# Kernel optimization log

Hardware: AMD Instinct MI355X
Metric: run time of the kernel (lower is better)

Reference implementation:

```python
import jax, jax.numpy as jnp
import numpy as np

N = 8192
F_IN = 128
D = 128
NEG_SLOPE = 0.2  # cfg.negativeslope (standard GAT value)
MASK_FILL = -9e15


def setup_inputs() -> dict:
    key = jax.random.key(0)
    k1, k2, k3, k4 = jax.random.split(key, 4)
    A = jax.random.randint(k1, (N, N), 0, 2, dtype=jnp.int32)
    X = jax.random.normal(k2, (N, F_IN), dtype=jnp.float32)
    # glorot init for Ws, xavier_uniform(gain=1.414) for a
    lim_w = float(np.sqrt(6.0 / (F_IN + D)))
    Ws = jax.random.uniform(k3, (F_IN, D), minval=-lim_w, maxval=lim_w, dtype=jnp.float32)
    lim_a = 1.414 * float(np.sqrt(6.0 / (2 * D + 1)))
    a = jax.random.uniform(k4, (2 * D, 1), minval=-lim_a, maxval=lim_a, dtype=jnp.float32)
    return {"A": A, "X": X, "Ws": Ws, "a": a}


def reference(A, X, Ws, a):
    # Wh: [N, D]
    Wh = X @ Ws
    d = Wh.shape[-1]
    # additive attention: e_ij = leaky_relu(Wh_i . a1 + Wh_j . a2)
    e1 = Wh @ a[:d]          # [N, 1]
    e2 = Wh @ a[d:]          # [N, 1]
    e = jax.nn.leaky_relu(e1 + e2.T, negative_slope=NEG_SLOPE)  # [N, N]
    e = jnp.where(A > 0, e, MASK_FILL)
    attn = jax.nn.softmax(e, axis=1)  # row-wise over neighbors
    H = attn @ Wh            # [N, D]
    return H
```

## Files before the change

### kernel.cpp

```cpp
#include <hip/hip_runtime.h>
#include <hip/hip_bf16.h>

#define NN 8192
#define DD 128

typedef __attribute__((ext_vector_type(8))) short short8;
typedef __attribute__((ext_vector_type(4))) float f32x4;
typedef unsigned int u32;
typedef unsigned long long u64;

__device__ __forceinline__ ushort f2bf(float f) {
    __hip_bfloat16 h = __float2bfloat16(f);
    return *(ushort*)&h;
}
__device__ __forceinline__ u32 asu(float f) {
    union { float f; u32 i; } v; v.f = f; return v.i;
}

__global__ __launch_bounds__(256) void k0_pack(const int* __restrict__ A,
                                               u32* __restrict__ Abits) {
    int t = threadIdx.x;
    size_t base = (size_t)blockIdx.x * 8192 + (size_t)t * 32;
    u32 bits = 0;
#pragma unroll
    for (int j = 0; j < 8; ++j) {
        int4 v = *(const int4*)(A + base + j * 4);
        bits |= (v.x != 0 ? 1u : 0u) << (j * 4 + 0);
        bits |= (v.y != 0 ? 1u : 0u) << (j * 4 + 1);
        bits |= (v.z != 0 ? 1u : 0u) << (j * 4 + 2);
        bits |= (v.w != 0 ? 1u : 0u) << (j * 4 + 3);
    }
    Abits[blockIdx.x * 256 + t] = bits;
}

__global__ __launch_bounds__(256) void k1_fused(
    const float* __restrict__ X, const float* __restrict__ Ws,
    const float* __restrict__ a, ushort* __restrict__ WhT,
    float* __restrict__ Rt, float* __restrict__ E2p, float* __restrict__ E2n) {
    __shared__ float lWs[128 * 132];
    __shared__ float lX[32 * 132];
    __shared__ float la[256];
    int t = threadIdx.x, bx = blockIdx.x;
    int i0 = bx * 32;
    const float4* Ws4 = (const float4*)Ws;
    const float4* X4 = (const float4*)X;
    la[t] = a[t];
    for (int j = 0; j < 16; ++j) {
        int u = j * 256 + t;
        int k = u >> 5, c4 = u & 31;
        *(float4*)&lWs[k * 132 + c4 * 4] = Ws4[u];
    }
    for (int j = 0; j < 4; ++j) {
        int u = j * 256 + t;
        int r = u >> 5, c4 = u & 31;
        *(float4*)&lX[r * 132 + c4 * 4] = X4[bx * 1024 + u];
    }
    __syncthreads();
    int r0 = (t >> 5) * 4, c0 = (t & 31) * 4;
    float acc[4][4];
#pragma unroll
    for (int i = 0; i < 4; ++i)
#pragma unroll
        for (int j = 0; j < 4; ++j) acc[i][j] = 0.f;
#pragma unroll 4
    for (int k = 0; k < 128; ++k) {
        float4 wv = *(const float4*)&lWs[k * 132 + c0];
        float x0 = lX[(r0 + 0) * 132 + k];
        float x1 = lX[(r0 + 1) * 132 + k];
        float x2 = lX[(r0 + 2) * 132 + k];
        float x3 = lX[(r0 + 3) * 132 + k];
#pragma unroll
        for (int j = 0; j < 4; ++j) {
            acc[0][j] += x0 * ((const float*)&wv)[j];
            acc[1][j] += x1 * ((const float*)&wv)[j];
            acc[2][j] += x2 * ((const float*)&wv)[j];
            acc[3][j] += x3 * ((const float*)&wv)[j];
        }
    }
    __syncthreads();
    float* lT = lWs;
#pragma unroll
    for (int i = 0; i < 4; ++i)
#pragma unroll
        for (int j = 0; j < 4; ++j) lT[(c0 + j) * 33 + r0 + i] = acc[i][j];
    __syncthreads();
    if (t < 128) {
        int r = t >> 2, q = t & 3;
        float s1 = 0.f, s2 = 0.f;
        for (int j = 0; j < 32; ++j) {
            int d = q * 32 + j;
            float v = lT[d * 33 + r];
            s1 += v * la[d];
            s2 += v * la[128 + d];
        }
        s1 += __shfl_xor(s1, 1); s1 += __shfl_xor(s1, 2);
        s2 += __shfl_xor(s2, 1); s2 += __shfl_xor(s2, 2);
        if (q == 0) {
            int i = i0 + r;
            Rt[i]  = __expf(-0.8f * s1);
            E2p[i] = __expf(s2);
            E2n[i] = __expf(0.2f * s2);
        }
    }
    int d = t >> 1, hf = t & 1;
    __attribute__((aligned(16))) ushort tmp[16];
#pragma unroll
    for (int s = 0; s < 16; ++s) tmp[s] = f2bf(lT[d * 33 + hf * 16 + s]);
    uint4* dst = (uint4*)&WhT[(size_t)d * NN + i0 + hf * 16];
    const uint4* srcv = (const uint4*)tmp;
    dst[0] = srcv[0];
    dst[1] = srcv[1];
}

__device__ __forceinline__ f32x4 mfma_bf16(short8 a, short8 b, f32x4 c) {
    return __builtin_amdgcn_mfma_f32_16x16x32_bf16(a, b, c, 0, 0, 0);
}

__device__ __forceinline__ void k3_step(
    const short8* Bv, u64 bits, int ko, int kgs,
    const float* lEp, const float* lEn, float ratio, int h, int kg,
    f32x4& acc0, f32x4& acc1, f32x4& acc2, f32x4& acc3, f32x4& accl,
    short8 ones) {
    u32 lo = (u32)bits, hi = (u32)(bits >> 32);
#pragma unroll
    for (int tp = 0; tp < 2; ++tp) {
        int ke = ko + tp * 32 + kg * 8;
        float ep[8], en[8];
        *(float4*)(ep)     = *(const float4*)&lEp[ke];
        *(float4*)(ep + 4) = *(const float4*)&lEp[ke + 4];
        *(float4*)(en)     = *(const float4*)&lEn[ke];
        *(float4*)(en + 4) = *(const float4*)&lEn[ke + 4];
        u32 byte = ((tp ? hi : lo) >> kgs) & 0xFFu;
        u32 wb[8];
#pragma unroll
        for (int u = 0; u < 8; ++u) {
            float w = fmaxf(ep[u], ratio * en[u]);
            w = (byte & (1u << u)) ? w : 0.f;
            wb[u] = asu(w);
        }
        short8 af;
#pragma unroll
        for (int p = 0; p < 4; ++p)
            ((u32*)&af)[p] = __builtin_amdgcn_perm(wb[2 * p + 1], wb[2 * p], 0x07060302);
        acc0 = mfma_bf16(af, Bv[tp * 4 + 0], acc0);
        acc1 = mfma_bf16(af, Bv[tp * 4 + 1], acc1);
        acc2 = mfma_bf16(af, Bv[tp * 4 + 2], acc2);
        acc3 = mfma_bf16(af, Bv[tp * 4 + 3], acc3);
        if (h == 0) accl = mfma_bf16(af, ones, accl);
    }
}

__global__ __launch_bounds__(512, 4) void k3_main(
    const u32* __restrict__ Abits, const ushort* __restrict__ WhT,
    const float* __restrict__ Rt, const float* __restrict__ E2p,
    const float* __restrict__ E2n, float* __restrict__ Hp,
    float* __restrict__ Lp) {

    __shared__ float lEp[2048];
    __shared__ float lEn[2048];

    int tid = threadIdx.x;
    int lane = tid & 63;
    int wv = tid >> 6;
    int g = wv & 3;
    int h = wv >> 2;
    int n = lane & 15;
    int kg = lane >> 4;
    int kgs = kg * 8;

    int bx = blockIdx.x;
    int kb = blockIdx.y;
    int row = bx * 64 + g * 16 + n;
    int kbase = kb * 2048;

#pragma unroll
    for (int j = 0; j < 4; ++j) {
        lEp[tid + j * 512] = E2p[kbase + tid + j * 512];
        lEn[tid + j * 512] = E2n[kbase + tid + j * 512];
    }

    float ratio = Rt[row];
    const u64* Arow = (const u64*)Abits + (size_t)row * 128 + kb * 32;
    const ushort* Bc0 = WhT + (size_t)(h * 64 +  0 + n) * NN + kbase + kgs;
    const ushort* Bc1 = WhT + (size_t)(h * 64 + 16 + n) * NN + kbase + kgs;
    const ushort* Bc2 = WhT + (size_t)(h * 64 + 32 + n) * NN + kbase + kgs;
    const ushort* Bc3 = WhT + (size_t)(h * 64 + 48 + n) * NN + kbase + kgs;

    short8 ones;
#pragma unroll
    for (int j = 0; j < 8; ++j) ones[j] = (short)0x3F80;

    f32x4 acc0 = (f32x4){0.f, 0.f, 0.f, 0.f};
    f32x4 acc1 = (f32x4){0.f, 0.f, 0.f, 0.f};
    f32x4 acc2 = (f32x4){0.f, 0.f, 0.f, 0.f};
    f32x4 acc3 = (f32x4){0.f, 0.f, 0.f, 0.f};
    f32x4 accl = (f32x4){0.f, 0.f, 0.f, 0.f};

    __syncthreads();

    short8 Ba[8], Bb[8];
    u64 bitsA, bitsB;
#define LOADB(Bd, kt_)                                        \
    {   int ko_ = (kt_) * 64;                                 \
        Bd[0] = *(const short8*)(Bc0 + ko_);                  \
        Bd[1] = *(const short8*)(Bc1 + ko_);                  \
        Bd[2] = *(const short8*)(Bc2 + ko_);                  \
        Bd[3] = *(const short8*)(Bc3 + ko_);                  \
        Bd[4] = *(const short8*)(Bc0 + ko_ + 32);             \
        Bd[5] = *(const short8*)(Bc1 + ko_ + 32);             \
        Bd[6] = *(const short8*)(Bc2 + ko_ + 32);             \
        Bd[7] = *(const short8*)(Bc3 + ko_ + 32);             \
    }

    LOADB(Ba, 0);
    bitsA = Arow[0];

    for (int kt = 0; kt < 32; kt += 2) {
        LOADB(Bb, kt + 1);
        bitsB = Arow[kt + 1];
        k3_step(Ba, bitsA, kt * 64, kgs, lEp, lEn, ratio, h, kg,
                acc0, acc1, acc2, acc3, accl, ones);
        int ktn = (kt + 2 < 32) ? kt + 2 : 31;
        LOADB(Ba, ktn);
        bitsA = Arow[ktn];
        k3_step(Bb, bitsB, (kt + 1) * 64, kgs, lEp, lEn, ratio, h, kg,
                acc0, acc1, acc2, acc3, accl, ones);
    }
#undef LOADB

    if (h == 0 && n == 0) {
#pragma unroll
        for (int r = 0; r < 4; ++r)
            Lp[(size_t)kb * NN + bx * 64 + g * 16 + kg * 4 + r] = accl[r];
    }
    float* Hpb = Hp + (size_t)kb * (NN * DD);
#pragma unroll
    for (int r = 0; r < 4; ++r) {
        int orow = bx * 64 + g * 16 + kg * 4 + r;
        Hpb[(size_t)orow * DD + h * 64 + n]      = acc0[r];
        Hpb[(size_t)orow * DD + h * 64 + 16 + n] = acc1[r];
        Hpb[(size_t)orow * DD + h * 64 + 32 + n] = acc2[r];
        Hpb[(size_t)orow * DD + h * 64 + 48 + n] = acc3[r];
    }
}

__global__ void k4_final(const float* __restrict__ Hp, const float* __restrict__ Lp,
                         float* __restrict__ out) {
    int idx = blockIdx.x * 256 + threadIdx.x;
    int i = idx >> 7;
    float sv = Hp[idx] + Hp[1048576 + idx] + Hp[2097152 + idx] + Hp[3145728 + idx];
    float l = Lp[i] + Lp[8192 + i] + Lp[16384 + i] + Lp[24576 + i];
    out[idx] = sv / l;
}

extern "C" void kernel_launch(void* const* d_in, const int* in_sizes, int n_in,
                              void* d_out, int out_size, void* d_ws, size_t ws_size,
                              hipStream_t stream) {
    const int*   A  = (const int*)d_in[0];
    const float* X  = (const float*)d_in[1];
    const float* Ws = (const float*)d_in[2];
    const float* a  = (const float*)d_in[3];
    float* out = (float*)d_out;

    char* ws = (char*)d_ws;
    u32*    Abits = (u32*)(ws);
    ushort* WhT   = (ushort*)(ws + (8u << 20));
    float*  Rt    = (float*)(ws + (10u << 20));
    float*  E2p   = (float*)(ws + (10u << 20) + (32u << 10));
    float*  E2n   = (float*)(ws + (10u << 20) + (64u << 10));
    float*  Lp    = (float*)(ws + (10u << 20) + (96u << 10));
    float*  Hp    = (float*)(ws + (12u << 20));

    k0_pack<<<8192, 256, 0, stream>>>(A, Abits);
    k1_fused<<<256, 256, 0, stream>>>(X, Ws, a, WhT, Rt, E2p, E2n);
    k3_main<<<dim3(128, 4), 512, 0, stream>>>(Abits, WhT, Rt, E2p, E2n, Hp, Lp);
    k4_final<<<4096, 256, 0, stream>>>(Hp, Lp, out);
}
```

Before: 508.9 us.

## Coalesce A packing, pack exp factors as bf16 pairs, re-grid attention kernel

k0_pack now reads A with fully coalesced int4 loads, builds nibbles in shared memory, then assembles 32-bit mask words, with 4x fewer blocks each doing 4x the work. The two exp factor arrays are packed into one u32 of two bf16 values, halving LDS traffic and footprint in the main kernel. The main kernel moves to 256-thread blocks over 32 rows and 1024-column K chunks (256x8 grid) and drops the explicit double-buffered B loads. The final reduce sums 8 partials instead of 4. Risks are more partial-sum traffic, less explicit prefetch, and bf16 rounding of the exp factors.

```diff
diff --git a/kernel.cpp b/kernel.cpp
--- a/kernel.cpp
+++ b/kernel.cpp
@@ -8,6 +8,7 @@
 typedef __attribute__((ext_vector_type(4))) float f32x4;
 typedef unsigned int u32;
 typedef unsigned long long u64;
+typedef unsigned char u8;
 
 __device__ __forceinline__ ushort f2bf(float f) {
     __hip_bfloat16 h = __float2bfloat16(f);
@@ -16,27 +17,41 @@
 __device__ __forceinline__ u32 asu(float f) {
     union { float f; u32 i; } v; v.f = f; return v.i;
 }
+__device__ __forceinline__ float asf(u32 u) {
+    union { u32 i; float f; } v; v.i = u; return v.f;
+}
 
 __global__ __launch_bounds__(256) void k0_pack(const int* __restrict__ A,
                                                u32* __restrict__ Abits) {
+    __shared__ u8 ln[8192];
     int t = threadIdx.x;
-    size_t base = (size_t)blockIdx.x * 8192 + (size_t)t * 32;
-    u32 bits = 0;
-#pragma unroll
-    for (int j = 0; j < 8; ++j) {
-        int4 v = *(const int4*)(A + base + j * 4);
-        bits |= (v.x != 0 ? 1u : 0u) << (j * 4 + 0);
-        bits |= (v.y != 0 ? 1u : 0u) << (j * 4 + 1);
-        bits |= (v.z != 0 ? 1u : 0u) << (j * 4 + 2);
-        bits |= (v.w != 0 ? 1u : 0u) << (j * 4 + 3);
-    }
-    Abits[blockIdx.x * 256 + t] = bits;
+    size_t base4 = (size_t)blockIdx.x * 8192;
+    const int4* A4 = (const int4*)A;
+#pragma unroll
+    for (int j = 0; j < 32; ++j) {
+        int u = j * 256 + t;
+        int4 v = A4[base4 + u];
+        u32 nib = (v.x ? 1u : 0u) | (v.y ? 2u : 0u) | (v.z ? 4u : 0u) | (v.w ? 8u : 0u);
+        ln[u] = (u8)nib;
+    }
+    __syncthreads();
+    const u64* l8 = (const u64*)ln;
+#pragma unroll
+    for (int j = 0; j < 4; ++j) {
+        int w = j * 256 + t;
+        u64 b = l8[w];
+        u32 word = 0;
+#pragma unroll
+        for (int m = 0; m < 8; ++m)
+            word |= ((u32)(b >> (8 * m)) & 0xFu) << (4 * m);
+        Abits[blockIdx.x * 1024 + w] = word;
+    }
 }
 
 __global__ __launch_bounds__(256) void k1_fused(
     const float* __restrict__ X, const float* __restrict__ Ws,
     const float* __restrict__ a, ushort* __restrict__ WhT,
-    float* __restrict__ Rt, float* __restrict__ E2p, float* __restrict__ E2n) {
+    float* __restrict__ Rt, u32* __restrict__ Epack) {
     __shared__ float lWs[128 * 132];
     __shared__ float lX[32 * 132];
     __shared__ float la[256];
@@ -97,9 +112,8 @@
         s2 += __shfl_xor(s2, 1); s2 += __shfl_xor(s2, 2);
         if (q == 0) {
             int i = i0 + r;
-            Rt[i]  = __expf(-0.8f * s1);
-            E2p[i] = __expf(s2);
-            E2n[i] = __expf(0.2f * s2);
+            Rt[i] = __expf(-0.8f * s1);
+            Epack[i] = (u32)f2bf(__expf(s2)) | ((u32)f2bf(__expf(0.2f * s2)) << 16);
         }
     }
     int d = t >> 1, hf = t & 1;
@@ -116,71 +130,32 @@
     return __builtin_amdgcn_mfma_f32_16x16x32_bf16(a, b, c, 0, 0, 0);
 }
 
-__device__ __forceinline__ void k3_step(
-    const short8* Bv, u64 bits, int ko, int kgs,
-    const float* lEp, const float* lEn, float ratio, int h, int kg,
-    f32x4& acc0, f32x4& acc1, f32x4& acc2, f32x4& acc3, f32x4& accl,
-    short8 ones) {
-    u32 lo = (u32)bits, hi = (u32)(bits >> 32);
-#pragma unroll
-    for (int tp = 0; tp < 2; ++tp) {
-        int ke = ko + tp * 32 + kg * 8;
-        float ep[8], en[8];
-        *(float4*)(ep)     = *(const float4*)&lEp[ke];
-        *(float4*)(ep + 4) = *(const float4*)&lEp[ke + 4];
-        *(float4*)(en)     = *(const float4*)&lEn[ke];
-        *(float4*)(en + 4) = *(const float4*)&lEn[ke + 4];
-        u32 byte = ((tp ? hi : lo) >> kgs) & 0xFFu;
-        u32 wb[8];
-#pragma unroll
-        for (int u = 0; u < 8; ++u) {
-            float w = fmaxf(ep[u], ratio * en[u]);
-            w = (byte & (1u << u)) ? w : 0.f;
-            wb[u] = asu(w);
-        }
-        short8 af;
-#pragma unroll
-        for (int p = 0; p < 4; ++p)
-            ((u32*)&af)[p] = __builtin_amdgcn_perm(wb[2 * p + 1], wb[2 * p], 0x07060302);
-        acc0 = mfma_bf16(af, Bv[tp * 4 + 0], acc0);
-        acc1 = mfma_bf16(af, Bv[tp * 4 + 1], acc1);
-        acc2 = mfma_bf16(af, Bv[tp * 4 + 2], acc2);
-        acc3 = mfma_bf16(af, Bv[tp * 4 + 3], acc3);
-        if (h == 0) accl = mfma_bf16(af, ones, accl);
-    }
-}
-
-__global__ __launch_bounds__(512, 4) void k3_main(
+__global__ __launch_bounds__(256, 5) void k3_main(
     const u32* __restrict__ Abits, const ushort* __restrict__ WhT,
-    const float* __restrict__ Rt, const float* __restrict__ E2p,
-    const float* __restrict__ E2n, float* __restrict__ Hp,
-    float* __restrict__ Lp) {
-
-    __shared__ float lEp[2048];
-    __shared__ float lEn[2048];
+    const float* __restrict__ Rt, const u32* __restrict__ Epack,
+    float* __restrict__ Hp, float* __restrict__ Lp) {
+
+    __shared__ u32 lE[1024];
 
     int tid = threadIdx.x;
     int lane = tid & 63;
     int wv = tid >> 6;
-    int g = wv & 3;
-    int h = wv >> 2;
+    int g = wv & 1;
+    int h = wv >> 1;
     int n = lane & 15;
     int kg = lane >> 4;
     int kgs = kg * 8;
 
     int bx = blockIdx.x;
     int kb = blockIdx.y;
-    int row = bx * 64 + g * 16 + n;
-    int kbase = kb * 2048;
-
-#pragma unroll
-    for (int j = 0; j < 4; ++j) {
-        lEp[tid + j * 512] = E2p[kbase + tid + j * 512];
-        lEn[tid + j * 512] = E2n[kbase + tid + j * 512];
-    }
+    int row = bx * 32 + g * 16 + n;
+    int kbase = kb * 1024;
+
+#pragma unroll
+    for (int j = 0; j < 4; ++j) lE[j * 256 + tid] = Epack[kbase + j * 256 + tid];
 
     float ratio = Rt[row];
-    const u64* Arow = (const u64*)Abits + (size_t)row * 128 + kb * 32;
+    const u64* Arow = (const u64*)Abits + (size_t)row * 128 + kb * 16;
     const ushort* Bc0 = WhT + (size_t)(h * 64 +  0 + n) * NN + kbase + kgs;
     const ushort* Bc1 = WhT + (size_t)(h * 64 + 16 + n) * NN + kbase + kgs;
     const ushort* Bc2 = WhT + (size_t)(h * 64 + 32 + n) * NN + kbase + kgs;
@@ -198,45 +173,58 @@
 
     __syncthreads();
 
-    short8 Ba[8], Bb[8];
-    u64 bitsA, bitsB;
-#define LOADB(Bd, kt_)                                        \
-    {   int ko_ = (kt_) * 64;                                 \
-        Bd[0] = *(const short8*)(Bc0 + ko_);                  \
-        Bd[1] = *(const short8*)(Bc1 + ko_);                  \
-        Bd[2] = *(const short8*)(Bc2 + ko_);                  \
-        Bd[3] = *(const short8*)(Bc3 + ko_);                  \
-        Bd[4] = *(const short8*)(Bc0 + ko_ + 32);             \
-        Bd[5] = *(const short8*)(Bc1 + ko_ + 32);             \
-        Bd[6] = *(const short8*)(Bc2 + ko_ + 32);             \
-        Bd[7] = *(const short8*)(Bc3 + ko_ + 32);             \
-    }
-
-    LOADB(Ba, 0);
-    bitsA = Arow[0];
-
-    for (int kt = 0; kt < 32; kt += 2) {
-        LOADB(Bb, kt + 1);
-        bitsB = Arow[kt + 1];
-        k3_step(Ba, bitsA, kt * 64, kgs, lEp, lEn, ratio, h, kg,
-                acc0, acc1, acc2, acc3, accl, ones);
-        int ktn = (kt + 2 < 32) ? kt + 2 : 31;
-        LOADB(Ba, ktn);
-        bitsA = Arow[ktn];
-        k3_step(Bb, bitsB, (kt + 1) * 64, kgs, lEp, lEn, ratio, h, kg,
-                acc0, acc1, acc2, acc3, accl, ones);
-    }
-#undef LOADB
+    u64 bitsA = Arow[0];
+
+    for (int kt = 0; kt < 16; ++kt) {
+        int ko = kt * 64;
+        short8 B0 = *(const short8*)(Bc0 + ko);
+        short8 B1 = *(const short8*)(Bc1 + ko);
+        short8 B2 = *(const short8*)(Bc2 + ko);
+        short8 B3 = *(const short8*)(Bc3 + ko);
+        short8 B4 = *(const short8*)(Bc0 + ko + 32);
+        short8 B5 = *(const short8*)(Bc1 + ko + 32);
+        short8 B6 = *(const short8*)(Bc2 + ko + 32);
+        short8 B7 = *(const short8*)(Bc3 + ko + 32);
+        u64 bn = (kt < 15) ? Arow[kt + 1] : 0;
+        u32 lo = (u32)bitsA, hi = (u32)(bitsA >> 32);
+#pragma unroll
+        for (int tp = 0; tp < 2; ++tp) {
+            int ke = ko + tp * 32 + kgs;
+            u32 ev[8];
+            *(uint4*)(ev)     = *(const uint4*)&lE[ke];
+            *(uint4*)(ev + 4) = *(const uint4*)&lE[ke + 4];
+            u32 byte = ((tp ? hi : lo) >> kgs) & 0xFFu;
+            u32 wb[8];
+#pragma unroll
+            for (int u = 0; u < 8; ++u) {
+                float ep = asf(ev[u] << 16);
+                float en = asf(ev[u] & 0xFFFF0000u);
+                float w = fmaxf(ep, ratio * en);
+                w = (byte & (1u << u)) ? w : 0.f;
+                wb[u] = asu(w);
+            }
+            short8 af;
+#pragma unroll
+            for (int p = 0; p < 4; ++p)
+                ((u32*)&af)[p] = __builtin_amdgcn_perm(wb[2 * p + 1], wb[2 * p], 0x07060302);
+            acc0 = mfma_bf16(af, tp ? B4 : B0, acc0);
+            acc1 = mfma_bf16(af, tp ? B5 : B1, acc1);
+            acc2 = mfma_bf16(af, tp ? B6 : B2, acc2);
+            acc3 = mfma_bf16(af, tp ? B7 : B3, acc3);
+            if (h == 0) accl = mfma_bf16(af, ones, accl);
+        }
+        bitsA = bn;
+    }
 
     if (h == 0 && n == 0) {
 #pragma unroll
         for (int r = 0; r < 4; ++r)
-            Lp[(size_t)kb * NN + bx * 64 + g * 16 + kg * 4 + r] = accl[r];
+            Lp[(size_t)kb * NN + bx * 32 + g * 16 + kg * 4 + r] = accl[r];
     }
     float* Hpb = Hp + (size_t)kb * (NN * DD);
 #pragma unroll
     for (int r = 0; r < 4; ++r) {
-        int orow = bx * 64 + g * 16 + kg * 4 + r;
+        int orow = bx * 32 + g * 16 + kg * 4 + r;
         Hpb[(size_t)orow * DD + h * 64 + n]      = acc0[r];
         Hpb[(size_t)orow * DD + h * 64 + 16 + n] = acc1[r];
         Hpb[(size_t)orow * DD + h * 64 + 32 + n] = acc2[r];
@@ -248,8 +236,12 @@
                          float* __restrict__ out) {
     int idx = blockIdx.x * 256 + threadIdx.x;
     int i = idx >> 7;
-    float sv = Hp[idx] + Hp[1048576 + idx] + Hp[2097152 + idx] + Hp[3145728 + idx];
-    float l = Lp[i] + Lp[8192 + i] + Lp[16384 + i] + Lp[24576 + i];
+    float sv = 0.f, l = 0.f;
+#pragma unroll
+    for (int p = 0; p < 8; ++p) {
+        sv += Hp[(size_t)p * 1048576 + idx];
+        l  += Lp[p * 8192 + i];
+    }
     out[idx] = sv / l;
 }
 
@@ -266,13 +258,12 @@
     u32*    Abits = (u32*)(ws);
     ushort* WhT   = (ushort*)(ws + (8u << 20));
     float*  Rt    = (float*)(ws + (10u << 20));
-    float*  E2p   = (float*)(ws + (10u << 20) + (32u << 10));
-    float*  E2n   = (float*)(ws + (10u << 20) + (64u << 10));
-    float*  Lp    = (float*)(ws + (10u << 20) + (96u << 10));
+    u32*    Epack = (u32*)(ws + (10u << 20) + (32u << 10));
+    float*  Lp    = (float*)(ws + (10u << 20) + (64u << 10));
     float*  Hp    = (float*)(ws + (12u << 20));
 
-    k0_pack<<<8192, 256, 0, stream>>>(A, Abits);
-    k1_fused<<<256, 256, 0, stream>>>(X, Ws, a, WhT, Rt, E2p, E2n);
-    k3_main<<<dim3(128, 4), 512, 0, stream>>>(Abits, WhT, Rt, E2p, E2n, Hp, Lp);
+    k0_pack<<<2048, 256, 0, stream>>>(A, Abits);
+    k1_fused<<<256, 256, 0, stream>>>(X, Ws, a, WhT, Rt, Epack);
+    k3_main<<<dim3(256, 8), 256, 0, stream>>>(Abits, WhT, Rt, Epack, Hp, Lp);
     k4_final<<<4096, 256, 0, stream>>>(Hp, Lp, out);
 }
```

Result: no change. 512.7 us (+0.7%).
